# Kernel tuning notes

Hardware: AMD Instinct MI355X
Metric: run time of the kernel (lower is better)

## Reference

```python
import jax, jax.numpy as jnp
import numpy as np

N_NODES = 50000
N_EDGES = 800000
D_IN, D_HID, D_OUT = 128, 128, 64


def _gcn_conv(x, row, col, W, b, num_nodes):
    # Linear (no bias in lin; bias added after aggregation)
    h = x @ W  # [N, d_out]
    # degree over destination (col), includes self-loops
    deg = jax.ops.segment_sum(jnp.ones_like(col, dtype=h.dtype), col, num_segments=num_nodes)
    dis = jnp.where(deg > 0, deg ** -0.5, 0.0)  # deg^{-1/2}, inf -> 0
    norm = dis[row] * dis[col]  # [E+N]
    msg = h[row] * norm[:, None]  # gather + scale
    out = jax.ops.segment_sum(msg, col, num_segments=num_nodes)  # scatter-add
    return out + b


def setup_inputs() -> dict:
    key = jax.random.key(0)
    k1, k2, k3, k4 = jax.random.split(key, 4)
    x = jax.random.normal(k1, (N_NODES, D_IN), dtype=jnp.float32)
    edge_index = jax.random.randint(k2, (2, N_EDGES), 0, N_NODES, dtype=jnp.int32)
    # glorot-like init for linear weights
    W1 = jax.random.normal(k3, (D_IN, D_HID), dtype=jnp.float32) * (2.0 / (D_IN + D_HID)) ** 0.5
    W2 = jax.random.normal(k4, (D_HID, D_OUT), dtype=jnp.float32) * (2.0 / (D_HID + D_OUT)) ** 0.5
    b1 = jnp.zeros((D_HID,), dtype=jnp.float32)
    b2 = jnp.zeros((D_OUT,), dtype=jnp.float32)
    return {"x": x, "edge_index": edge_index, "W1": W1, "b1": b1, "W2": W2, "b2": b2}


def reference(x, edge_index, W1, b1, W2, b2):
    n = x.shape[0]
    # add self-loops
    loops = jnp.arange(n, dtype=edge_index.dtype)
    row = jnp.concatenate([edge_index[0], loops])
    col = jnp.concatenate([edge_index[1], loops])
    h = _gcn_conv(x, row, col, W1, b1, n)
    h = jax.nn.relu(h)  # dropout is identity in eval mode
    out = _gcn_conv(h, row, col, W2, b2, n)
    return out
```

## Files before the change

kernel.cpp:

```cpp
#include <hip/hip_runtime.h>

#define BSH 7
#define BMSK 127
#define NB 391
#define ROWSH 13
#define NCH 7
#define NBLKS 128
#define BINCAP 3072
#define SMAX1 768
#define SMAX2 1024

typedef __attribute__((ext_vector_type(8))) short short8;
typedef __attribute__((ext_vector_type(4))) float f32x4;
typedef __attribute__((ext_vector_type(4))) unsigned int u32x4;

static inline size_t alignup(size_t x) { return (x + 255) & ~(size_t)255; }

__device__ __forceinline__ unsigned short f2bf(float f) {
    unsigned int u = __float_as_uint(f);
    u = (u + 0x7fffu + ((u >> 16) & 1u)) >> 16;
    return (unsigned short)u;
}

__global__ __launch_bounds__(256) void k_prep(const float* __restrict__ W1,
                                              const float* __restrict__ W2,
                                              unsigned short* __restrict__ Wt1,
                                              unsigned short* __restrict__ Wt2) {
    int i = blockIdx.x * 256 + threadIdx.x;
    if (i < 128 * 128) { int k = i >> 7, c = i & 127; Wt1[(size_t)c * 128 + k] = f2bf(W1[i]); }
    if (i < 128 * 64)  { int k = i >> 6, c = i & 63;  Wt2[(size_t)c * 128 + k] = f2bf(W2[i]); }
}

__global__ __launch_bounds__(256) void k_front(const float* __restrict__ x,
                                               const unsigned short* __restrict__ Wt1,
                                               unsigned short* __restrict__ hs1, int M,
                                               const int* __restrict__ colp, int nE,
                                               unsigned* __restrict__ counts, int G1) {
    if ((int)blockIdx.x >= G1) {
        int blk = blockIdx.x - G1;
        __shared__ unsigned h[NB];
        for (int i = threadIdx.x; i < NB; i += 256) h[i] = 0;
        __syncthreads();
        int chunk = (nE + NBLKS - 1) / NBLKS;
        int e0 = blk * chunk, e1 = min(nE, e0 + chunk);
        for (int e = e0 + (int)threadIdx.x; e < e1; e += 256)
            atomicAdd(&h[colp[e] >> BSH], 1u);
        __syncthreads();
        for (int i = threadIdx.x; i < NB; i += 256) counts[(size_t)i * NBLKS + blk] = h[i];
        return;
    }
    const int NT = 8;
    const int lane = threadIdx.x & 63;
    const int wave = threadIdx.x >> 6;
    const int m0 = blockIdx.x * 64 + wave * 16;
    const int lrow = lane & 15;
    const int lk = lane >> 4;
    int arow = m0 + lrow;
    if (arow >= M) arow = M - 1;

    f32x4 acc[NT];
#pragma unroll
    for (int t = 0; t < NT; ++t) acc[t] = (f32x4){0.f, 0.f, 0.f, 0.f};

#pragma unroll
    for (int k0 = 0; k0 < 4; ++k0) {
        const int kb = k0 * 32 + lk * 8;
        const float* ap = &x[(size_t)arow * 128 + kb];
        f32x4 v0 = __builtin_nontemporal_load((const f32x4*)ap);
        f32x4 v1 = __builtin_nontemporal_load((const f32x4*)(ap + 4));
        short8 afrag;
#pragma unroll
        for (int q = 0; q < 4; ++q) {
            afrag[q] = (short)f2bf(v0[q]);
            afrag[4 + q] = (short)f2bf(v1[q]);
        }
#pragma unroll
        for (int t = 0; t < NT; ++t) {
            const int bcol = t * 16 + lrow;
            short8 bfrag = *(const short8*)&Wt1[(size_t)bcol * 128 + kb];
            acc[t] = __builtin_amdgcn_mfma_f32_16x16x32_bf16(afrag, bfrag, acc[t], 0, 0, 0);
        }
    }
#pragma unroll
    for (int i = 0; i < 4; ++i) {
        int row = m0 + lk * 4 + i;
        if (row < M) {
#pragma unroll
            for (int t = 0; t < NT; ++t)
                hs1[(size_t)row * 128 + t * 16 + lrow] = f2bf(acc[t][i]);
        }
    }
}

__global__ __launch_bounds__(NBLKS) void k_scanA(unsigned* __restrict__ counts,
                                                 unsigned* __restrict__ bintot) {
    int bin = blockIdx.x, t = threadIdx.x;
    __shared__ unsigned ps[NBLKS];
    unsigned s = counts[(size_t)bin * NBLKS + t];
    ps[t] = s;
    __syncthreads();
    for (int d = 1; d < NBLKS; d <<= 1) {
        unsigned v = (t >= d) ? ps[t - d] : 0u;
        __syncthreads();
        ps[t] += v;
        __syncthreads();
    }
    counts[(size_t)bin * NBLKS + t] = ps[t] - s;
    if (t == NBLKS - 1) bintot[bin] = ps[NBLKS - 1];
}

__global__ __launch_bounds__(256) void k_scatter(const int* __restrict__ colp,
                                                 const int* __restrict__ rowp, int nE,
                                                 const unsigned* __restrict__ counts,
                                                 const unsigned* __restrict__ bintot,
                                                 unsigned* __restrict__ pairs,
                                                 unsigned* __restrict__ edgebase) {
    __shared__ unsigned bb[NB];
    __shared__ unsigned ts[256];
    int t = threadIdx.x, blk = blockIdx.x;
    for (int i = t; i < NB; i += 256) bb[i] = bintot[i];
    __syncthreads();
    const int CH = (NB + 255) / 256;
    unsigned s = 0;
    unsigned own[CH];
#pragma unroll
    for (int j = 0; j < CH; ++j) {
        int idx = t * CH + j;
        unsigned v = (idx < NB) ? bb[idx] : 0u;
        own[j] = s; s += v;
    }
    ts[t] = s;
    __syncthreads();
    for (int d = 1; d < 256; d <<= 1) {
        unsigned v = (t >= d) ? ts[t - d] : 0u;
        __syncthreads();
        ts[t] += v;
        __syncthreads();
    }
    unsigned base = ts[t] - s;
    __syncthreads();
#pragma unroll
    for (int j = 0; j < CH; ++j) {
        int idx = t * CH + j;
        if (idx < NB) bb[idx] = base + own[j];
    }
    __syncthreads();
    if (blk == 0) {
        for (int b = t; b < NB; b += 256) edgebase[b] = bb[b];
        if (t == 0) edgebase[NB] = (unsigned)nE;
    }
    for (int i = t; i < NB; i += 256) bb[i] += counts[(size_t)i * NBLKS + blk];
    __syncthreads();
    int chunk = (nE + NBLKS - 1) / NBLKS;
    int e0 = blk * chunk, e1 = min(nE, e0 + chunk);
    for (int e = e0 + (int)t; e < e1; e += 256) {
        int c = colp[e], r = rowp[e];
        unsigned pos = atomicAdd(&bb[c >> BSH], 1u);
        pairs[pos] = ((unsigned)r << BSH) | (unsigned)(c & BMSK);
    }
}

__global__ __launch_bounds__(256) void k_binbuild(const unsigned* __restrict__ pairs,
                                                  const unsigned* __restrict__ edgebase,
                                                  unsigned* __restrict__ csr,
                                                  unsigned* __restrict__ off,
                                                  float* __restrict__ dis, int n) {
    __shared__ unsigned lp[BINCAP];
    __shared__ unsigned lr[BINCAP];
    __shared__ unsigned hist[128 * NCH];
    __shared__ unsigned scn[256];
    int b = blockIdx.x, t = threadIdx.x;
    unsigned e0 = edgebase[b], e1 = edgebase[b + 1];
    unsigned ec = e1 - e0;
    if (ec > BINCAP) ec = BINCAP;
    for (int i = t; i < 128 * NCH; i += 256) hist[i] = 0;
    __syncthreads();
    for (unsigned i = t; i < ec; i += 256) {
        unsigned v = pairs[e0 + i];
        lp[i] = v;
        unsigned key = (v & BMSK) * NCH + ((v >> BSH) >> ROWSH);
        atomicAdd(&hist[key], 1u);
    }
    __syncthreads();
    const int HCH = 4;
    unsigned own[HCH];
    unsigned s = 0;
#pragma unroll
    for (int j = 0; j < HCH; ++j) {
        int idx = t * HCH + j;
        unsigned v = (idx < 128 * NCH) ? hist[idx] : 0u;
        own[j] = s; s += v;
    }
    scn[t] = s;
    __syncthreads();
    for (int d = 1; d < 256; d <<= 1) {
        unsigned v = (t >= d) ? scn[t - d] : 0u;
        __syncthreads();
        scn[t] += v;
        __syncthreads();
    }
    unsigned base = scn[t] - s;
    __syncthreads();
#pragma unroll
    for (int j = 0; j < HCH; ++j) {
        int idx = t * HCH + j;
        if (idx < 128 * NCH) hist[idx] = base + own[j];
    }
    __syncthreads();
    if (t < 128) {
        int node = (b << BSH) + t;
        if (node < n) {
            unsigned start = hist[t * NCH];
            unsigned next = (t == 127) ? ec : hist[(t + 1) * NCH];
            off[node] = e0 + start;
            dis[node] = rsqrtf((float)(next - start + 1));
        }
    }
    if (b == NB - 1 && t == 0) off[n] = e1;
    __syncthreads();
    for (unsigned i = t; i < ec; i += 256) {
        unsigned v = lp[i];
        unsigned key = (v & BMSK) * NCH + ((v >> BSH) >> ROWSH);
        unsigned pos = atomicAdd(&hist[key], 1u);
        lr[pos] = v >> BSH;
    }
    __syncthreads();
    for (unsigned i = t; i < ec; i += 256) csr[e0 + i] = lr[i];
}

__device__ __forceinline__ void acc8s(float a[8], u32x4 u, float d) {
    a[0] = fmaf(__uint_as_float(u[0] << 16), d, a[0]);
    a[1] = fmaf(__uint_as_float(u[0] & 0xffff0000u), d, a[1]);
    a[2] = fmaf(__uint_as_float(u[1] << 16), d, a[2]);
    a[3] = fmaf(__uint_as_float(u[1] & 0xffff0000u), d, a[3]);
    a[4] = fmaf(__uint_as_float(u[2] << 16), d, a[4]);
    a[5] = fmaf(__uint_as_float(u[2] & 0xffff0000u), d, a[5]);
    a[6] = fmaf(__uint_as_float(u[3] << 16), d, a[6]);
    a[7] = fmaf(__uint_as_float(u[3] & 0xffff0000u), d, a[7]);
}

__device__ __forceinline__ void acc8(float a[8], u32x4 u) {
    a[0] += __uint_as_float(u[0] << 16);
    a[1] += __uint_as_float(u[0] & 0xffff0000u);
    a[2] += __uint_as_float(u[1] << 16);
    a[3] += __uint_as_float(u[1] & 0xffff0000u);
    a[4] += __uint_as_float(u[2] << 16);
    a[5] += __uint_as_float(u[2] & 0xffff0000u);
    a[6] += __uint_as_float(u[3] << 16);
    a[7] += __uint_as_float(u[3] & 0xffff0000u);
}

__global__ __launch_bounds__(256) void k_fuse2(const unsigned short* __restrict__ hs1,
                                               const unsigned* __restrict__ csr,
                                               const unsigned* __restrict__ off,
                                               const float* __restrict__ dis,
                                               const float* __restrict__ b1,
                                               const unsigned short* __restrict__ Wt2,
                                               unsigned short* __restrict__ hs2, int n) {
    __shared__ unsigned short st[16 * 136];
    __shared__ unsigned sc_csr[SMAX1];
    __shared__ float sc_dis[SMAX1];
    const int tid = threadIdx.x;
    int vloc = tid >> 4;
    int c = tid & 15;
    int blk16 = blockIdx.x * 16;
    int v = blk16 + vloc;
    if (v >= n) v = n - 1;

    unsigned s0 = off[blk16 < n ? blk16 : n - 1];
    unsigned eend = off[(blk16 + 16 < n) ? blk16 + 16 : n];
    unsigned cnt = eend - s0;
    if (cnt > SMAX1) cnt = SMAX1;
    for (unsigned i = tid; i < cnt; i += 256) {
        unsigned r = csr[s0 + i];
        sc_csr[i] = r;
        sc_dis[i] = dis[r];
    }
    __syncthreads();

    const u32x4* h4 = (const u32x4*)hs1;
    size_t base = (size_t)v * 16 + c;
    unsigned ls = off[v] - s0, le = off[v + 1] - s0;
    float dv = dis[v];

    float a[8];
#pragma unroll
    for (int j = 0; j < 8; ++j) a[j] = 0.f;
    acc8s(a, h4[base], dv);

    if (le <= SMAX1) {
        unsigned i = ls;
        for (; i + 8 <= le; i += 8) {
            unsigned r[8];
            float d[8];
            u32x4 m[8];
#pragma unroll
            for (int j = 0; j < 8; ++j) { r[j] = sc_csr[i + j]; d[j] = sc_dis[i + j]; }
#pragma unroll
            for (int j = 0; j < 8; ++j) m[j] = h4[(size_t)r[j] * 16 + c];
#pragma unroll
            for (int j = 0; j < 8; ++j) acc8s(a, m[j], d[j]);
        }
        for (; i < le; ++i)
            acc8s(a, h4[(size_t)sc_csr[i] * 16 + c], sc_dis[i]);
    } else {
        for (unsigned i = ls; i < le; ++i) {
            unsigned r = csr[s0 + i];
            acc8s(a, h4[(size_t)r * 16 + c], dis[r]);
        }
    }

    u32x4 pk;
#pragma unroll
    for (int q = 0; q < 4; ++q) {
        float lo = fmaxf(a[2 * q] * dv + b1[c * 8 + 2 * q], 0.f);
        float hi = fmaxf(a[2 * q + 1] * dv + b1[c * 8 + 2 * q + 1], 0.f);
        pk[q] = (unsigned)f2bf(lo) | ((unsigned)f2bf(hi) << 16);
    }
    *(u32x4*)&st[vloc * 136 + c * 8] = pk;
    __syncthreads();

    const int lane = tid & 63;
    const int wave = tid >> 6;
    const int lrow = lane & 15;
    const int lk = lane >> 4;
    f32x4 acc = (f32x4){0.f, 0.f, 0.f, 0.f};
#pragma unroll
    for (int k0 = 0; k0 < 4; ++k0) {
        const int kb = k0 * 32 + lk * 8;
        short8 afrag = *(const short8*)&st[lrow * 136 + kb];
        const int bcol = wave * 16 + lrow;
        short8 bfrag = *(const short8*)&Wt2[(size_t)bcol * 128 + kb];
        acc = __builtin_amdgcn_mfma_f32_16x16x32_bf16(afrag, bfrag, acc, 0, 0, 0);
    }
#pragma unroll
    for (int i2 = 0; i2 < 4; ++i2) {
        int row = blk16 + lk * 4 + i2;
        if (row < n) {
            float sc = dis[row];
            hs2[(size_t)row * 64 + wave * 16 + lrow] = f2bf(acc[i2] * sc);
        }
    }
}

__global__ __launch_bounds__(256) void k_gather2(const unsigned short* __restrict__ hs,
                                                 const unsigned* __restrict__ csr,
                                                 const unsigned* __restrict__ off,
                                                 const float* __restrict__ dis,
                                                 const float* __restrict__ bias,
                                                 float* __restrict__ outp, int n) {
    __shared__ unsigned sc_csr[SMAX2];
    const int tid = threadIdx.x;
    int blk32 = blockIdx.x * 32;
    int v = blk32 + (tid >> 3);
    int c = tid & 7;
    bool live = (v < n);
    if (!live) v = n - 1;

    unsigned s0 = off[blk32 < n ? blk32 : n - 1];
    unsigned eend = off[(blk32 + 32 < n) ? blk32 + 32 : n];
    unsigned cnt = eend - s0;
    if (cnt > SMAX2) cnt = SMAX2;
    for (unsigned i = tid; i < cnt; i += 256) sc_csr[i] = csr[s0 + i];
    __syncthreads();
    if (!live) return;

    const u32x4* h4 = (const u32x4*)hs;
    size_t base = (size_t)v * 8 + c;
    unsigned ls = off[v] - s0, le = off[v + 1] - s0;
    float dv = dis[v];

    float a[8];
#pragma unroll
    for (int j = 0; j < 8; ++j) a[j] = 0.f;
    acc8(a, h4[base]);

    if (le <= SMAX2) {
        unsigned i = ls;
        for (; i + 8 <= le; i += 8) {
            unsigned r[8];
            u32x4 m[8];
#pragma unroll
            for (int j = 0; j < 8; ++j) r[j] = sc_csr[i + j];
#pragma unroll
            for (int j = 0; j < 8; ++j) m[j] = h4[(size_t)r[j] * 8 + c];
#pragma unroll
            for (int j = 0; j < 8; ++j) acc8(a, m[j]);
        }
        for (; i < le; ++i) acc8(a, h4[(size_t)sc_csr[i] * 8 + c]);
    } else {
        for (unsigned i = ls; i < le; ++i) acc8(a, h4[(size_t)csr[s0 + i] * 8 + c]);
    }

    float rr[8];
#pragma unroll
    for (int j = 0; j < 8; ++j) rr[j] = a[j] * dv + bias[c * 8 + j];
    f32x4 lov = {rr[0], rr[1], rr[2], rr[3]};
    f32x4 hiv = {rr[4], rr[5], rr[6], rr[7]};
    __builtin_nontemporal_store(lov, (f32x4*)&outp[(size_t)v * 64 + c * 8]);
    __builtin_nontemporal_store(hiv, (f32x4*)&outp[(size_t)v * 64 + c * 8 + 4]);
}

extern "C" void kernel_launch(void* const* d_in, const int* in_sizes, int n_in,
                              void* d_out, int out_size, void* d_ws, size_t ws_size,
                              hipStream_t stream) {
    const float* x  = (const float*)d_in[0];
    const int*   ei = (const int*)d_in[1];
    const float* W1 = (const float*)d_in[2];
    const float* b1 = (const float*)d_in[3];
    const float* W2 = (const float*)d_in[4];
    const float* b2 = (const float*)d_in[5];

    const int Din = 128;
    const int Nn = in_sizes[0] / Din;
    const int E  = in_sizes[1] / 2;
    const int* rowp = ei;
    const int* colp = ei + E;

    char* ws = (char*)d_ws;
    size_t off_ = 0;
    unsigned*       counts   = (unsigned*)(ws + off_);       off_ = alignup(off_ + (size_t)NB * NBLKS * 4);
    unsigned*       bintot   = (unsigned*)(ws + off_);       off_ = alignup(off_ + (size_t)NB * 4);
    unsigned*       edgebase = (unsigned*)(ws + off_);       off_ = alignup(off_ + (size_t)(NB + 1) * 4);
    unsigned*       pairs    = (unsigned*)(ws + off_);       off_ = alignup(off_ + (size_t)E * 4);
    unsigned*       csr      = (unsigned*)(ws + off_);       off_ = alignup(off_ + (size_t)E * 4);
    unsigned*       offv     = (unsigned*)(ws + off_);       off_ = alignup(off_ + (size_t)(Nn + 1) * 4);
    float*          dis      = (float*)(ws + off_);          off_ = alignup(off_ + (size_t)Nn * 4);
    unsigned short* Wt1      = (unsigned short*)(ws + off_); off_ = alignup(off_ + 128 * 128 * 2);
    unsigned short* Wt2      = (unsigned short*)(ws + off_); off_ = alignup(off_ + 128 * 64 * 2);
    unsigned short* hs1      = (unsigned short*)(ws + off_); off_ = alignup(off_ + (size_t)Nn * 128 * 2);
    unsigned short* hs2      = (unsigned short*)(ws + off_); off_ = alignup(off_ + (size_t)Nn * 64 * 2);
    float*          outp     = (float*)d_out;

    const int G1 = (Nn + 63) / 64;

    k_prep<<<64, 256, 0, stream>>>(W1, W2, Wt1, Wt2);
    k_front<<<G1 + NBLKS, 256, 0, stream>>>(x, Wt1, hs1, Nn, colp, E, counts, G1);
    k_scanA<<<NB, NBLKS, 0, stream>>>(counts, bintot);
    k_scatter<<<NBLKS, 256, 0, stream>>>(colp, rowp, E, counts, bintot, pairs, edgebase);
    k_binbuild<<<NB, 256, 0, stream>>>(pairs, edgebase, csr, offv, dis, Nn);

    k_fuse2<<<(Nn + 15) / 16, 256, 0, stream>>>(hs1, csr, offv, dis, b1, Wt2, hs2, Nn);

    k_gather2<<<(Nn + 31) / 32, 256, 0, stream>>>(hs2, csr, offv, dis, b2, outp, Nn);
}
```

Before: 110.5 us.

## Fold bin scan into scatter and split CSR bin build across two blocks

Result: slower. 116.3 us (+5.2%).

```diff
diff --git a/kernel.cpp b/kernel.cpp
--- a/kernel.cpp
+++ b/kernel.cpp
@@ -7,6 +7,7 @@
 #define NCH 7
 #define NBLKS 128
 #define BINCAP 3072
+#define HCAP 1792
 #define SMAX1 768
 #define SMAX2 1024
 
@@ -92,42 +93,31 @@
     }
 }
 
-__global__ __launch_bounds__(NBLKS) void k_scanA(unsigned* __restrict__ counts,
-                                                 unsigned* __restrict__ bintot) {
-    int bin = blockIdx.x, t = threadIdx.x;
-    __shared__ unsigned ps[NBLKS];
-    unsigned s = counts[(size_t)bin * NBLKS + t];
-    ps[t] = s;
-    __syncthreads();
-    for (int d = 1; d < NBLKS; d <<= 1) {
-        unsigned v = (t >= d) ? ps[t - d] : 0u;
-        __syncthreads();
-        ps[t] += v;
-        __syncthreads();
-    }
-    counts[(size_t)bin * NBLKS + t] = ps[t] - s;
-    if (t == NBLKS - 1) bintot[bin] = ps[NBLKS - 1];
-}
-
 __global__ __launch_bounds__(256) void k_scatter(const int* __restrict__ colp,
                                                  const int* __restrict__ rowp, int nE,
                                                  const unsigned* __restrict__ counts,
-                                                 const unsigned* __restrict__ bintot,
                                                  unsigned* __restrict__ pairs,
                                                  unsigned* __restrict__ edgebase) {
     __shared__ unsigned bb[NB];
     __shared__ unsigned ts[256];
     int t = threadIdx.x, blk = blockIdx.x;
-    for (int i = t; i < NB; i += 256) bb[i] = bintot[i];
-    __syncthreads();
     const int CH = (NB + 255) / 256;
+    unsigned own[CH], mypre[CH];
     unsigned s = 0;
-    unsigned own[CH];
 #pragma unroll
     for (int j = 0; j < CH; ++j) {
         int idx = t * CH + j;
-        unsigned v = (idx < NB) ? bb[idx] : 0u;
-        own[j] = s; s += v;
+        unsigned tot = 0, pr = 0;
+        if (idx < NB) {
+            const unsigned* row = &counts[(size_t)idx * NBLKS];
+#pragma unroll 4
+            for (int b = 0; b < NBLKS; ++b) {
+                unsigned v = row[b];
+                tot += v;
+                pr += (b < blk) ? v : 0u;
+            }
+        }
+        own[j] = s; mypre[j] = pr; s += tot;
     }
     ts[t] = s;
     __syncthreads();
@@ -138,7 +128,6 @@
         __syncthreads();
     }
     unsigned base = ts[t] - s;
-    __syncthreads();
 #pragma unroll
     for (int j = 0; j < CH; ++j) {
         int idx = t * CH + j;
@@ -149,7 +138,12 @@
         for (int b = t; b < NB; b += 256) edgebase[b] = bb[b];
         if (t == 0) edgebase[NB] = (unsigned)nE;
     }
-    for (int i = t; i < NB; i += 256) bb[i] += counts[(size_t)i * NBLKS + blk];
+    __syncthreads();
+#pragma unroll
+    for (int j = 0; j < CH; ++j) {
+        int idx = t * CH + j;
+        if (idx < NB) bb[idx] += mypre[j];
+    }
     __syncthreads();
     int chunk = (nE + NBLKS - 1) / NBLKS;
     int e0 = blk * chunk, e1 = min(nE, e0 + chunk);
@@ -165,33 +159,64 @@
                                                   unsigned* __restrict__ csr,
                                                   unsigned* __restrict__ off,
                                                   float* __restrict__ dis, int n) {
-    __shared__ unsigned lp[BINCAP];
-    __shared__ unsigned lr[BINCAP];
-    __shared__ unsigned hist[128 * NCH];
+    __shared__ unsigned lp[HCAP];
+    __shared__ unsigned lr[HCAP];
+    __shared__ unsigned hist[64 * NCH];
     __shared__ unsigned scn[256];
-    int b = blockIdx.x, t = threadIdx.x;
+    int bh = blockIdx.x, t = threadIdx.x;
+    int b = bh >> 1, half = bh & 1;
     unsigned e0 = edgebase[b], e1 = edgebase[b + 1];
     unsigned ec = e1 - e0;
     if (ec > BINCAP) ec = BINCAP;
-    for (int i = t; i < 128 * NCH; i += 256) hist[i] = 0;
-    __syncthreads();
-    for (unsigned i = t; i < ec; i += 256) {
-        unsigned v = pairs[e0 + i];
-        lp[i] = v;
-        unsigned key = (v & BMSK) * NCH + ((v >> BSH) >> ROWSH);
-        atomicAdd(&hist[key], 1u);
-    }
-    __syncthreads();
-    const int HCH = 4;
-    unsigned own[HCH];
-    unsigned s = 0;
+    for (int i = t; i < 64 * NCH; i += 256) hist[i] = 0;
+    __syncthreads();
+
+    unsigned vals[12];
+    bool keep[12];
+    unsigned nkeep = 0;
+#pragma unroll
+    for (int j = 0; j < 12; ++j) {
+        unsigned i = (unsigned)t + (unsigned)j * 256u;
+        bool ok = (i < ec);
+        unsigned v = ok ? pairs[e0 + i] : 0u;
+        bool kp = ok && (((v >> 6) & 1u) == (unsigned)half);
+        vals[j] = v;
+        keep[j] = kp;
+        if (kp) {
+            ++nkeep;
+            atomicAdd(&hist[(v & 63u) * NCH + ((v >> BSH) >> ROWSH)], 1u);
+        }
+    }
+    scn[t] = nkeep;
+    __syncthreads();
+    for (int d = 1; d < 256; d <<= 1) {
+        unsigned v = (t >= d) ? scn[t - d] : 0u;
+        __syncthreads();
+        scn[t] += v;
+        __syncthreads();
+    }
+    unsigned wbase = scn[t] - nkeep;
+    unsigned nmine = scn[255];
+    if (nmine > HCAP) nmine = HCAP;
+    __syncthreads();
+#pragma unroll
+    for (int j = 0; j < 12; ++j) {
+        if (keep[j]) {
+            if (wbase < HCAP) lp[wbase] = vals[j];
+            ++wbase;
+        }
+    }
+
+    const int HCH = 2;
+    unsigned hown[HCH];
+    unsigned hs = 0;
 #pragma unroll
     for (int j = 0; j < HCH; ++j) {
         int idx = t * HCH + j;
-        unsigned v = (idx < 128 * NCH) ? hist[idx] : 0u;
-        own[j] = s; s += v;
-    }
-    scn[t] = s;
+        unsigned v = (idx < 64 * NCH) ? hist[idx] : 0u;
+        hown[j] = hs; hs += v;
+    }
+    scn[t] = hs;
     __syncthreads();
     for (int d = 1; d < 256; d <<= 1) {
         unsigned v = (t >= d) ? scn[t - d] : 0u;
@@ -199,33 +224,36 @@
         scn[t] += v;
         __syncthreads();
     }
-    unsigned base = scn[t] - s;
+    unsigned hbase = scn[t] - hs;
     __syncthreads();
 #pragma unroll
     for (int j = 0; j < HCH; ++j) {
         int idx = t * HCH + j;
-        if (idx < 128 * NCH) hist[idx] = base + own[j];
-    }
-    __syncthreads();
-    if (t < 128) {
-        int node = (b << BSH) + t;
+        if (idx < 64 * NCH) hist[idx] = hbase + hown[j];
+    }
+    __syncthreads();
+
+    unsigned cbase = half ? (ec - nmine) : 0u;
+    if (t < 64) {
+        int node = (b << BSH) + half * 64 + t;
         if (node < n) {
             unsigned start = hist[t * NCH];
-            unsigned next = (t == 127) ? ec : hist[(t + 1) * NCH];
-            off[node] = e0 + start;
+            unsigned next = (t == 63) ? nmine : hist[(t + 1) * NCH];
+            off[node] = e0 + cbase + start;
             dis[node] = rsqrtf((float)(next - start + 1));
         }
     }
-    if (b == NB - 1 && t == 0) off[n] = e1;
-    __syncthreads();
-    for (unsigned i = t; i < ec; i += 256) {
+    if (b == NB - 1 && half == 1 && t == 0) off[n] = e1;
+    __syncthreads();
+
+    for (unsigned i = t; i < nmine; i += 256) {
         unsigned v = lp[i];
-        unsigned key = (v & BMSK) * NCH + ((v >> BSH) >> ROWSH);
+        unsigned key = (v & 63u) * NCH + ((v >> BSH) >> ROWSH);
         unsigned pos = atomicAdd(&hist[key], 1u);
-        lr[pos] = v >> BSH;
-    }
-    __syncthreads();
-    for (unsigned i = t; i < ec; i += 256) csr[e0 + i] = lr[i];
+        if (pos < HCAP) lr[pos] = v >> BSH;
+    }
+    __syncthreads();
+    for (unsigned i = t; i < nmine; i += 256) csr[e0 + cbase + i] = lr[i];
 }
 
 __device__ __forceinline__ void acc8s(float a[8], u32x4 u, float d) {
@@ -420,7 +448,6 @@
     char* ws = (char*)d_ws;
     size_t off_ = 0;
     unsigned*       counts   = (unsigned*)(ws + off_);       off_ = alignup(off_ + (size_t)NB * NBLKS * 4);
-    unsigned*       bintot   = (unsigned*)(ws + off_);       off_ = alignup(off_ + (size_t)NB * 4);
     unsigned*       edgebase = (unsigned*)(ws + off_);       off_ = alignup(off_ + (size_t)(NB + 1) * 4);
     unsigned*       pairs    = (unsigned*)(ws + off_);       off_ = alignup(off_ + (size_t)E * 4);
     unsigned*       csr      = (unsigned*)(ws + off_);       off_ = alignup(off_ + (size_t)E * 4);
@@ -436,9 +463,8 @@
 
     k_prep<<<64, 256, 0, stream>>>(W1, W2, Wt1, Wt2);
     k_front<<<G1 + NBLKS, 256, 0, stream>>>(x, Wt1, hs1, Nn, colp, E, counts, G1);
-    k_scanA<<<NB, NBLKS, 0, stream>>>(counts, bintot);
-    k_scatter<<<NBLKS, 256, 0, stream>>>(colp, rowp, E, counts, bintot, pairs, edgebase);
-    k_binbuild<<<NB, 256, 0, stream>>>(pairs, edgebase, csr, offv, dis, Nn);
+    k_scatter<<<NBLKS, 256, 0, stream>>>(colp, rowp, E, counts, pairs, edgebase);
+    k_binbuild<<<2 * NB, 256, 0, stream>>>(pairs, edgebase, csr, offv, dis, Nn);
 
     k_fuse2<<<(Nn + 15) / 16, 256, 0, stream>>>(hs1, csr, offv, dis, b1, Wt2, hs2, Nn);
 
```
